# Kernel tuning notes

Hardware: AMD Instinct MI355X
Metric: run time of the kernel (lower is better)

The kernel has to match this reference:

```python
import jax, jax.numpy as jnp
import numpy as np

B, N, F = 32, 64, 128          # batch, num_nodes, n_in_node
K, H, M, NH = 4, 256, 256, 256 # edge_types, msg_hid, msg_out, n_hid
E = N * (N - 1)                # fully-connected directed edges = 4032


def setup_inputs() -> dict:
    key = jax.random.key(0)
    ks = jax.random.split(key, 12)
    inputs = jax.random.normal(ks[0], (B, N, F), dtype=jnp.float32)
    # soft edge-type assignment per edge (rows sum to 1, as in NRI)
    rel_type = jax.nn.softmax(jax.random.normal(ks[1], (B, E, K), dtype=jnp.float32), axis=-1)
    # one-hot receiver/sender matrices for all i != j pairs
    idx = np.array([(i, j) for i in range(N) for j in range(N) if i != j], dtype=np.int64)
    eye = np.eye(N, dtype=np.float32)
    rel_rec = jnp.asarray(eye[idx[:, 0]])   # [E, N]
    rel_send = jnp.asarray(eye[idx[:, 1]])  # [E, N]
    # per-edge-type message MLP weights (stacked over K): y = x @ W + b
    W1 = jax.random.normal(ks[2], (K, 2 * F, H), dtype=jnp.float32) / np.sqrt(2 * F)
    b1 = jnp.zeros((K, H), dtype=jnp.float32)
    W2 = jax.random.normal(ks[3], (K, H, M), dtype=jnp.float32) / np.sqrt(H)
    b2 = jnp.zeros((K, M), dtype=jnp.float32)
    # output MLP
    Wo1 = jax.random.normal(ks[4], (F + M, NH), dtype=jnp.float32) / np.sqrt(F + M)
    bo1 = jnp.zeros((NH,), dtype=jnp.float32)
    Wo2 = jax.random.normal(ks[5], (NH, NH), dtype=jnp.float32) / np.sqrt(NH)
    bo2 = jnp.zeros((NH,), dtype=jnp.float32)
    Wo3 = jax.random.normal(ks[6], (NH, F), dtype=jnp.float32) / np.sqrt(NH)
    bo3 = jnp.zeros((F,), dtype=jnp.float32)
    return {"inputs": inputs, "rel_type": rel_type, "rel_rec": rel_rec, "rel_send": rel_send,
            "W1": W1, "b1": b1, "W2": W2, "b2": b2,
            "Wo1": Wo1, "bo1": bo1, "Wo2": Wo2, "bo2": bo2, "Wo3": Wo3, "bo3": bo3}


def reference(inputs, rel_type, rel_rec, rel_send, W1, b1, W2, b2, Wo1, bo1, Wo2, bo2, Wo3, bo3):
    # gather node states to edges via one-hot matmul (as in the source)
    receivers = jnp.einsum('en,bnf->bef', rel_rec, inputs)   # [B,E,F]
    senders = jnp.einsum('en,bnf->bef', rel_send, inputs)    # [B,E,F]
    pre_msg = jnp.concatenate([receivers, senders], axis=-1)  # [B,E,2F]
    # per-edge-type 2-layer ReLU MLP, batched over the K edge types
    h = jax.nn.relu(jnp.einsum('bef,kfh->bkeh', pre_msg, W1) + b1[:, None, :])  # [B,K,E,H]
    msg = jax.nn.relu(jnp.einsum('bkeh,khm->bkem', h, W2) + b2[:, None, :])     # [B,K,E,M]
    # mask by soft edge type and accumulate over types (dropout p=0 -> identity)
    all_msgs = jnp.einsum('bkem,bek->bem', msg, rel_type)     # [B,E,M]
    # scatter-aggregate messages to receiver nodes via one-hot matmul
    agg_msgs = jnp.einsum('en,bem->bnm', rel_rec, all_msgs)   # [B,N,M]
    aug = jnp.concatenate([inputs, agg_msgs], axis=-1)        # [B,N,F+M]
    p = jax.nn.relu(aug @ Wo1 + bo1)
    p = jax.nn.relu(p @ Wo2 + bo2)
    p = p @ Wo3 + bo3
    return inputs + p
```

## Files before the change

kernel.cpp:

```cpp
#include <hip/hip_runtime.h>


#define B_ 32
#define N_ 64
#define F_ 128
#define K_ 4
#define E_ 4032

#define WS_W2T 0u
#define WS_R   524288u
#define WS_S   4718592u
#define WS_AGG 8912896u

typedef unsigned short u16;
typedef u16    u16x4  __attribute__((ext_vector_type(4)));
typedef u16    u16x8  __attribute__((ext_vector_type(8)));
typedef __bf16 bf16x8 __attribute__((ext_vector_type(8)));
typedef float  f32x4  __attribute__((ext_vector_type(4)));
typedef float  f32x16 __attribute__((ext_vector_type(16)));

__device__ __forceinline__ u16 f2bf(float f) {
    unsigned u; __builtin_memcpy(&u, &f, 4);
    return (u16)((u + 0x7FFFu + ((u >> 16) & 1u)) >> 16);
}
__device__ __forceinline__ float bf2f(u16 u) {
    unsigned v = ((unsigned)u) << 16;
    float f; __builtin_memcpy(&f, &v, 4); return f;
}
__device__ __forceinline__ void gl_lds16(const u16* g, u16* l) {
    __builtin_amdgcn_global_load_lds(
        (const __attribute__((address_space(1))) void*)g,
        (__attribute__((address_space(3))) void*)l, 16, 0, 0);
}

#define LBAR() do { \
    asm volatile("s_waitcnt lgkmcnt(0)" ::: "memory"); \
    __builtin_amdgcn_s_barrier(); \
    __builtin_amdgcn_sched_barrier(0); \
} while (0)

__global__ __launch_bounds__(256) void prep_rs_kernel(
    const float* __restrict__ W2, const float* __restrict__ x,
    const float* __restrict__ W1, const float* __restrict__ b1,
    u16* __restrict__ W2t, u16* __restrict__ R, u16* __restrict__ S)
{
    __shared__ u16 ldsA[64 * 136];
    __shared__ u16 ldsW[32 * 136];
    const int tid = threadIdx.x;

    if (blockIdx.x < 1024) {
        unsigned gid = blockIdx.x * 256u + tid;
        unsigned chunk = gid >> 13, r = gid & 8191u;
        unsigned g = r >> 11, n = (r >> 3) & 255u, e = r & 7u;
        unsigned k = chunk >> 3, kc = chunk & 7u, ks2 = g >> 1, lhh = g & 1u;
        unsigned kk = kc * 32u + ks2 * 16u + lhh * 8u + e;
        W2t[gid] = f2bf(W2[(k * 256u + kk) * 256u + n]);
        return;
    }

    const int lane = tid & 63, w = tid >> 6;
    const int quad = lane >> 4, mloc = lane & 15;
    const int bx = blockIdx.x - 1024;
    const int k = bx >> 6, half = (bx >> 5) & 1, b = bx & 31;

    for (int idx = tid; idx < 2048; idx += 256) {
        int row = idx >> 5, c4 = idx & 31;
        f32x4 v = *(const f32x4*)&x[(b * 64 + row) * 128 + c4 * 4];
        u16x4 o;
#pragma unroll
        for (int e = 0; e < 4; ++e) o[e] = f2bf(v[e]);
        *(u16x4*)&ldsA[row * 136 + c4 * 4] = o;
    }
    __syncthreads();

    bf16x8 aF[4];
#pragma unroll
    for (int ks = 0; ks < 4; ++ks)
        aF[ks] = *(const bf16x8*)&ldsA[(w * 16 + mloc) * 136 + quad * 8 + ks * 32];

    u16* dst = half ? S : R;
    for (int c = 0; c < 8; ++c) {
        __syncthreads();
        for (int idx = tid; idx < 4096; idx += 256) {
            int n = idx & 31, f = idx >> 5;
            ldsW[n * 136 + f] = f2bf(W1[(k * 256 + half * 128 + f) * 256 + c * 32 + n]);
        }
        __syncthreads();
#pragma unroll
        for (int nt = 0; nt < 2; ++nt) {
            f32x4 acc = (f32x4){0.f, 0.f, 0.f, 0.f};
            const int boff = (nt * 16 + mloc) * 136 + quad * 8;
#pragma unroll
            for (int ks = 0; ks < 4; ++ks)
                acc = __builtin_amdgcn_mfma_f32_16x16x32_bf16(
                    aF[ks], *(const bf16x8*)&ldsW[boff + ks * 32], acc, 0, 0, 0);
            const int n = c * 32 + nt * 16 + mloc;
            const float bias = half ? 0.f : b1[k * 256 + n];
#pragma unroll
            for (int r = 0; r < 4; ++r) {
                int row = w * 16 + quad * 4 + r;
                dst[(size_t)(k * 2048 + b * 64 + row) * 256 + n] = f2bf(acc[r] + bias);
            }
        }
    }
}

__global__ __launch_bounds__(256, 2) void edge6_kernel(
    const u16* __restrict__ R, const u16* __restrict__ S,
    const float* __restrict__ rel, const u16* __restrict__ W2t,
    const float* __restrict__ b2, u16* __restrict__ aggb)
{
    __shared__ u16   WtS[3][8192];
    __shared__ u16   HS[2][4][128][8];
    __shared__ float Rf[2][4][256];
    __shared__ float rtS[2][4][64];
    __shared__ float b2S[4][256];

    const int tid  = threadIdx.x;
    const int lane = tid & 63;
    const int w    = tid >> 6;
    const int l31  = lane & 31;
    const int lh   = lane >> 5;
    const int bid  = ((blockIdx.x & 7) << 7) | (blockIdx.x >> 3);
    const int b    = bid >> 5;
    const int i0   = (bid & 31) * 2;
    const int brow = tid >> 2;
    const int bc   = tid & 3;

#pragma unroll
    for (int g = 0; g < 4; ++g) {
        gl_lds16(W2t + g * 2048 + w * 512 + lane * 8,        &WtS[0][g * 2048 + w * 512]);
        gl_lds16(W2t + 8192 + g * 2048 + w * 512 + lane * 8, &WtS[1][g * 2048 + w * 512]);
    }
    for (int t = tid; t < 1024; t += 256) ((float*)b2S)[t] = b2[t];
    for (int t = tid; t < 512; t += 256) {
        int recv = t >> 8, rem = t & 255, k = rem >> 6, j = rem & 63;
        int i = i0 + recv;
        float v = 0.f;
        if (j != i) {
            int jj = j - (j > i);
            v = rel[((size_t)(b * E_) + i * 63 + jj) * 4 + k];
        }
        rtS[recv][k][j] = v;
    }
    {
        int recv = tid >> 7, k = (tid >> 5) & 3, e8 = tid & 31;
        u16x8 t8 = *(const u16x8*)&R[((size_t)(k * 2048 + b * 64 + i0 + recv)) * 256 + e8 * 8];
#pragma unroll
        for (int e = 0; e < 8; ++e) Rf[recv][k][e8 * 8 + e] = bf2f(t8[e]);
    }
    u16x8 sv = *(const u16x8*)&S[((size_t)(b * 64 + brow)) * 256 + bc * 8];
    __syncthreads();

    {
#pragma unroll
        for (int recv = 0; recv < 2; ++recv) {
            const float* rp = &Rf[recv][0][bc * 8];
            f32x4 r0 = *(const f32x4*)rp, r1 = *(const f32x4*)(rp + 4);
            bf16x8 o;
#pragma unroll
            for (int e = 0; e < 4; ++e) {
                o[e]     = (__bf16)fmaxf(r0[e] + bf2f(sv[e]),     0.f);
                o[4 + e] = (__bf16)fmaxf(r1[e] + bf2f(sv[4 + e]), 0.f);
            }
            *(bf16x8*)&HS[0][bc][recv * 64 + brow][0] = o;
        }
    }
    LBAR();

    float amsg[2][2] = {{0.f, 0.f}, {0.f, 0.f}};
    f32x16 acc[4][2];
    int sc = 0;

    for (int it = 0; it < 32; ++it) {
        const int kT = it >> 3, kcT = it & 7;
        if (kcT == 0) {
#pragma unroll
            for (int mt = 0; mt < 4; ++mt)
#pragma unroll
                for (int nt = 0; nt < 2; ++nt) acc[mt][nt] = (f32x16)(0.f);
        }
        u16x8 svN;
        if (it < 31) {
            const int kT2 = (it + 1) >> 3, kc2 = (it + 1) & 7;
            svN = *(const u16x8*)&S[((size_t)(kT2 * 2048 + b * 64 + brow)) * 256 + kc2 * 32 + bc * 8];
        }
        if (it < 30) {
            const int s2 = (sc < 1) ? sc + 2 : sc - 1;
            const u16* src = W2t + (size_t)(it + 2) * 8192;
            u16* dstb = &WtS[s2][0];
#pragma unroll
            for (int g = 0; g < 4; ++g)
                gl_lds16(src + g * 2048 + w * 512 + lane * 8, dstb + g * 2048 + w * 512);
        }
        if (it < 30)       { asm volatile("s_waitcnt vmcnt(9)" ::: "memory"); }
        else if (it == 30) { asm volatile("s_waitcnt vmcnt(5)" ::: "memory"); }
        else               { asm volatile("s_waitcnt vmcnt(0)" ::: "memory"); }
        __builtin_amdgcn_sched_barrier(0);

        const u16* buf = WtS[sc];
        const u16(*hs)[128][8] = HS[it & 1];
        __builtin_amdgcn_s_setprio(1);
#pragma unroll
        for (int ks2 = 0; ks2 < 2; ++ks2) {
            bf16x8 A[4], Bv[2];
#pragma unroll
            for (int mt = 0; mt < 4; ++mt)
                A[mt] = *(const bf16x8*)&hs[ks2 * 2 + lh][mt * 32 + l31][0];
#pragma unroll
            for (int nt = 0; nt < 2; ++nt)
                Bv[nt] = *(const bf16x8*)&buf[(ks2 * 2 + lh) * 2048 + (w * 64 + nt * 32 + l31) * 8];
#pragma unroll
            for (int mt = 0; mt < 4; ++mt)
#pragma unroll
                for (int nt = 0; nt < 2; ++nt)
                    acc[mt][nt] = __builtin_amdgcn_mfma_f32_32x32x16_bf16(A[mt], Bv[nt], acc[mt][nt], 0, 0, 0);
        }
        __builtin_amdgcn_s_setprio(0);

        if (it < 31) {
            const int kT2 = (it + 1) >> 3, kc2 = (it + 1) & 7;
            const int db = (it + 1) & 1;
#pragma unroll
            for (int recv = 0; recv < 2; ++recv) {
                const float* rp = &Rf[recv][kT2][kc2 * 32 + bc * 8];
                f32x4 r0 = *(const f32x4*)rp, r1 = *(const f32x4*)(rp + 4);
                bf16x8 o;
#pragma unroll
                for (int e = 0; e < 4; ++e) {
                    o[e]     = (__bf16)fmaxf(r0[e] + bf2f(svN[e]),     0.f);
                    o[4 + e] = (__bf16)fmaxf(r1[e] + bf2f(svN[4 + e]), 0.f);
                }
                *(bf16x8*)&HS[db][bc][recv * 64 + brow][0] = o;
            }
        }
        if (kcT == 7) {
#pragma unroll
            for (int nt = 0; nt < 2; ++nt) {
                const float bias = b2S[kT][w * 64 + nt * 32 + l31];
#pragma unroll
                for (int mt = 0; mt < 4; ++mt) {
                    const int recv = mt >> 1;
                    float s = 0.f;
#pragma unroll
                    for (int rq = 0; rq < 4; ++rq) {
                        f32x4 rt4 = *(const f32x4*)&rtS[recv][kT][(mt & 1) * 32 + rq * 8 + 4 * lh];
#pragma unroll
                        for (int e = 0; e < 4; ++e) {
                            float v = acc[mt][nt][rq * 4 + e] + bias;
                            v = v > 0.f ? v : 0.f;
                            s += rt4[e] * v;
                        }
                    }
                    amsg[recv][nt] += s;
                }
            }
        }
        LBAR();
        sc = (sc < 2) ? sc + 1 : 0;
    }

#pragma unroll
    for (int recv = 0; recv < 2; ++recv)
#pragma unroll
        for (int nt = 0; nt < 2; ++nt) {
            float s = amsg[recv][nt] + __shfl_xor(amsg[recv][nt], 32);
            if (lh == 0)
                aggb[(size_t)(b * 64 + i0 + recv) * 256 + w * 64 + nt * 32 + l31] = f2bf(s);
        }
}

__global__ __launch_bounds__(256) void outmlp3_kernel(
    const float* __restrict__ x, const u16* __restrict__ aggb,
    const float* __restrict__ Wo1, const float* __restrict__ bo1,
    const float* __restrict__ Wo2, const float* __restrict__ bo2,
    const float* __restrict__ Wo3, const float* __restrict__ bo3,
    float* __restrict__ out)
{
    __shared__ u16 wch[4][256][8];
    __shared__ u16 p1S[32 * 264];
    __shared__ u16 p2S[32 * 264];
    const int tid = threadIdx.x, lane = tid & 63, w = tid >> 6;
    const int quad = lane >> 4, mloc = lane & 15;
    const int row0 = blockIdx.x * 32;

    {
        f32x4 acc[2][4];
#pragma unroll
        for (int mt = 0; mt < 2; ++mt)
#pragma unroll
            for (int nt = 0; nt < 4; ++nt) acc[mt][nt] = (f32x4){0.f, 0.f, 0.f, 0.f};
        float wr[32];
#pragma unroll
        for (int g = 0; g < 4; ++g)
#pragma unroll
            for (int e = 0; e < 8; ++e) wr[g * 8 + e] = Wo1[(g * 8 + e) * 256 + tid];
        for (int kk = 0; kk < 12; ++kk) {
            bf16x8 aF[2];
#pragma unroll
            for (int mt = 0; mt < 2; ++mt) {
                const int row = row0 + mt * 16 + mloc;
                if (kk < 4) {
                    u16x8 t;
#pragma unroll
                    for (int e = 0; e < 8; ++e) t[e] = f2bf(x[row * 128 + kk * 32 + quad * 8 + e]);
                    __builtin_memcpy(&aF[mt], &t, 16);
                } else {
                    aF[mt] = *(const bf16x8*)&aggb[(size_t)row * 256 + (kk - 4) * 32 + quad * 8];
                }
            }
#pragma unroll
            for (int g = 0; g < 4; ++g) {
                u16x8 o;
#pragma unroll
                for (int e = 0; e < 8; ++e) o[e] = f2bf(wr[g * 8 + e]);
                *(u16x8*)&wch[g][tid][0] = o;
            }
            if (kk + 1 < 12) {
#pragma unroll
                for (int g = 0; g < 4; ++g)
#pragma unroll
                    for (int e = 0; e < 8; ++e) wr[g * 8 + e] = Wo1[((kk + 1) * 32 + g * 8 + e) * 256 + tid];
            }
            LBAR();
#pragma unroll
            for (int nt = 0; nt < 4; ++nt) {
                bf16x8 bF = *(const bf16x8*)&wch[quad][w * 64 + nt * 16 + mloc][0];
#pragma unroll
                for (int mt = 0; mt < 2; ++mt)
                    acc[mt][nt] = __builtin_amdgcn_mfma_f32_16x16x32_bf16(aF[mt], bF, acc[mt][nt], 0, 0, 0);
            }
            LBAR();
        }
#pragma unroll
        for (int nt = 0; nt < 4; ++nt) {
            const int n = w * 64 + nt * 16 + mloc;
            const float bias = bo1[n];
#pragma unroll
            for (int mt = 0; mt < 2; ++mt)
#pragma unroll
                for (int r = 0; r < 4; ++r) {
                    float v = acc[mt][nt][r] + bias;
                    p1S[(mt * 16 + quad * 4 + r) * 264 + n] = f2bf(v > 0.f ? v : 0.f);
                }
        }
    }
    LBAR();
    {
        f32x4 acc[2][4];
#pragma unroll
        for (int mt = 0; mt < 2; ++mt)
#pragma unroll
            for (int nt = 0; nt < 4; ++nt) acc[mt][nt] = (f32x4){0.f, 0.f, 0.f, 0.f};
        float wr[32];
#pragma unroll
        for (int g = 0; g < 4; ++g)
#pragma unroll
            for (int e = 0; e < 8; ++e) wr[g * 8 + e] = Wo2[(g * 8 + e) * 256 + tid];
        for (int kk = 0; kk < 8; ++kk) {
            bf16x8 aF[2];
#pragma unroll
            for (int mt = 0; mt < 2; ++mt)
                aF[mt] = *(const bf16x8*)&p1S[(mt * 16 + mloc) * 264 + kk * 32 + quad * 8];
#pragma unroll
            for (int g = 0; g < 4; ++g) {
                u16x8 o;
#pragma unroll
                for (int e = 0; e < 8; ++e) o[e] = f2bf(wr[g * 8 + e]);
                *(u16x8*)&wch[g][tid][0] = o;
            }
            if (kk + 1 < 8) {
#pragma unroll
                for (int g = 0; g < 4; ++g)
#pragma unroll
                    for (int e = 0; e < 8; ++e) wr[g * 8 + e] = Wo2[((kk + 1) * 32 + g * 8 + e) * 256 + tid];
            }
            LBAR();
#pragma unroll
            for (int nt = 0; nt < 4; ++nt) {
                bf16x8 bF = *(const bf16x8*)&wch[quad][w * 64 + nt * 16 + mloc][0];
#pragma unroll
                for (int mt = 0; mt < 2; ++mt)
                    acc[mt][nt] = __builtin_amdgcn_mfma_f32_16x16x32_bf16(aF[mt], bF, acc[mt][nt], 0, 0, 0);
            }
            LBAR();
        }
#pragma unroll
        for (int nt = 0; nt < 4; ++nt) {
            const int n = w * 64 + nt * 16 + mloc;
            const float bias = bo2[n];
#pragma unroll
            for (int mt = 0; mt < 2; ++mt)
#pragma unroll
                for (int r = 0; r < 4; ++r) {
                    float v = acc[mt][nt][r] + bias;
                    p2S[(mt * 16 + quad * 4 + r) * 264 + n] = f2bf(v > 0.f ? v : 0.f);
                }
        }
    }
    LBAR();
    {
        f32x4 acc[2][2];
#pragma unroll
        for (int mt = 0; mt < 2; ++mt)
#pragma unroll
            for (int nt = 0; nt < 2; ++nt) acc[mt][nt] = (f32x4){0.f, 0.f, 0.f, 0.f};
        const int sn = tid & 127, sh = tid >> 7;
        float wr[16];
#pragma unroll
        for (int g2 = 0; g2 < 2; ++g2)
#pragma unroll
            for (int e = 0; e < 8; ++e) wr[g2 * 8 + e] = Wo3[((sh * 2 + g2) * 8 + e) * 128 + sn];
        for (int kk = 0; kk < 8; ++kk) {
            bf16x8 aF[2];
#pragma unroll
            for (int mt = 0; mt < 2; ++mt)
                aF[mt] = *(const bf16x8*)&p2S[(mt * 16 + mloc) * 264 + kk * 32 + quad * 8];
#pragma unroll
            for (int g2 = 0; g2 < 2; ++g2) {
                const int g = sh * 2 + g2;
                u16x8 o;
#pragma unroll
                for (int e = 0; e < 8; ++e) o[e] = f2bf(wr[g2 * 8 + e]);
                *(u16x8*)&wch[g][sn][0] = o;
            }
            if (kk + 1 < 8) {
#pragma unroll
                for (int g2 = 0; g2 < 2; ++g2)
#pragma unroll
                    for (int e = 0; e < 8; ++e)
                        wr[g2 * 8 + e] = Wo3[((kk + 1) * 32 + (sh * 2 + g2) * 8 + e) * 128 + sn];
            }
            LBAR();
#pragma unroll
            for (int nt = 0; nt < 2; ++nt) {
                bf16x8 bF = *(const bf16x8*)&wch[quad][w * 32 + nt * 16 + mloc][0];
#pragma unroll
                for (int mt = 0; mt < 2; ++mt)
                    acc[mt][nt] = __builtin_amdgcn_mfma_f32_16x16x32_bf16(aF[mt], bF, acc[mt][nt], 0, 0, 0);
            }
            LBAR();
        }
#pragma unroll
        for (int nt = 0; nt < 2; ++nt) {
            const int n = w * 32 + nt * 16 + mloc;
            const float bias = bo3[n];
#pragma unroll
            for (int mt = 0; mt < 2; ++mt)
#pragma unroll
                for (int r = 0; r < 4; ++r) {
                    const int grow = row0 + mt * 16 + quad * 4 + r;
                    out[grow * 128 + n] = x[grow * 128 + n] + acc[mt][nt][r] + bias;
                }
        }
    }
}

extern "C" void kernel_launch(void* const* d_in, const int* in_sizes, int n_in,
                              void* d_out, int out_size, void* d_ws, size_t ws_size,
                              hipStream_t stream) {
    const float* x   = (const float*)d_in[0];
    const float* rel = (const float*)d_in[1];
    const float* W1  = (const float*)d_in[4];
    const float* b1  = (const float*)d_in[5];
    const float* W2  = (const float*)d_in[6];
    const float* b2  = (const float*)d_in[7];
    const float* Wo1 = (const float*)d_in[8];
    const float* bo1 = (const float*)d_in[9];
    const float* Wo2 = (const float*)d_in[10];
    const float* bo2 = (const float*)d_in[11];
    const float* Wo3 = (const float*)d_in[12];
    const float* bo3 = (const float*)d_in[13];
    float* out = (float*)d_out;

    char* ws = (char*)d_ws;
    u16* W2t  = (u16*)(ws + WS_W2T);
    u16* R    = (u16*)(ws + WS_R);
    u16* S    = (u16*)(ws + WS_S);
    u16* aggb = (u16*)(ws + WS_AGG);

    prep_rs_kernel<<<1280, 256, 0, stream>>>(W2, x, W1, b1, W2t, R, S);
    edge6_kernel<<<1024, 256, 0, stream>>>(R, S, rel, W2t, b2, aggb);
    outmlp3_kernel<<<64, 256, 0, stream>>>(x, aggb, Wo1, bo1, Wo2, bo2, Wo3, bo3, out);
}
```

Measured before the change: 224.2 us.

## Replace triple-buffered W2 prefetch with double-buffering and plain syncthreads

The edge kernel drops from a three-stage LDS ring for W2 tiles, prefetched two iterations ahead with explicit vmcnt waits, to a two-stage double buffer prefetched one iteration ahead. Synchronisation now uses __syncthreads instead of the custom barrier, and the s_setprio hints and sched_barrier are removed. The b2 bias is read from global memory rather than staged in LDS. This cuts LDS use, which may help occupancy or simplify scheduling. The cost is less latency hiding for the global-to-LDS loads, and the full barrier likely waits on all outstanding loads each iteration.

```diff
diff --git a/kernel.cpp b/kernel.cpp
--- a/kernel.cpp
+++ b/kernel.cpp
@@ -105,16 +105,15 @@
     }
 }
 
-__global__ __launch_bounds__(256, 2) void edge6_kernel(
+__global__ __launch_bounds__(256, 2) void edge7_kernel(
     const u16* __restrict__ R, const u16* __restrict__ S,
     const float* __restrict__ rel, const u16* __restrict__ W2t,
     const float* __restrict__ b2, u16* __restrict__ aggb)
 {
-    __shared__ u16   WtS[3][8192];
+    __shared__ u16   WtS[2][8192];
     __shared__ u16   HS[2][4][128][8];
     __shared__ float Rf[2][4][256];
     __shared__ float rtS[2][4][64];
-    __shared__ float b2S[4][256];
 
     const int tid  = threadIdx.x;
     const int lane = tid & 63;
@@ -127,12 +126,13 @@
     const int brow = tid >> 2;
     const int bc   = tid & 3;
 
-#pragma unroll
-    for (int g = 0; g < 4; ++g) {
-        gl_lds16(W2t + g * 2048 + w * 512 + lane * 8,        &WtS[0][g * 2048 + w * 512]);
-        gl_lds16(W2t + 8192 + g * 2048 + w * 512 + lane * 8, &WtS[1][g * 2048 + w * 512]);
-    }
-    for (int t = tid; t < 1024; t += 256) ((float*)b2S)[t] = b2[t];
+    {
+        const u16* src = W2t + w * 2048;
+        u16* dst = &WtS[0][w * 2048];
+#pragma unroll
+        for (int it2 = 0; it2 < 4; ++it2)
+            gl_lds16(src + it2 * 512 + lane * 8, dst + it2 * 512);
+    }
     for (int t = tid; t < 512; t += 256) {
         int recv = t >> 8, rem = t & 255, k = rem >> 6, j = rem & 63;
         int i = i0 + recv;
@@ -166,11 +166,10 @@
             *(bf16x8*)&HS[0][bc][recv * 64 + brow][0] = o;
         }
     }
-    LBAR();
+    __syncthreads();
 
     float amsg[2][2] = {{0.f, 0.f}, {0.f, 0.f}};
     f32x16 acc[4][2];
-    int sc = 0;
 
     for (int it = 0; it < 32; ++it) {
         const int kT = it >> 3, kcT = it & 7;
@@ -182,25 +181,16 @@
         }
         u16x8 svN;
         if (it < 31) {
+            const u16* src = W2t + (size_t)(it + 1) * 8192 + w * 2048;
+            u16* dst = &WtS[(it + 1) & 1][w * 2048];
+#pragma unroll
+            for (int it2 = 0; it2 < 4; ++it2)
+                gl_lds16(src + it2 * 512 + lane * 8, dst + it2 * 512);
             const int kT2 = (it + 1) >> 3, kc2 = (it + 1) & 7;
             svN = *(const u16x8*)&S[((size_t)(kT2 * 2048 + b * 64 + brow)) * 256 + kc2 * 32 + bc * 8];
         }
-        if (it < 30) {
-            const int s2 = (sc < 1) ? sc + 2 : sc - 1;
-            const u16* src = W2t + (size_t)(it + 2) * 8192;
-            u16* dstb = &WtS[s2][0];
-#pragma unroll
-            for (int g = 0; g < 4; ++g)
-                gl_lds16(src + g * 2048 + w * 512 + lane * 8, dstb + g * 2048 + w * 512);
-        }
-        if (it < 30)       { asm volatile("s_waitcnt vmcnt(9)" ::: "memory"); }
-        else if (it == 30) { asm volatile("s_waitcnt vmcnt(5)" ::: "memory"); }
-        else               { asm volatile("s_waitcnt vmcnt(0)" ::: "memory"); }
-        __builtin_amdgcn_sched_barrier(0);
-
-        const u16* buf = WtS[sc];
+        const u16* buf = WtS[it & 1];
         const u16(*hs)[128][8] = HS[it & 1];
-        __builtin_amdgcn_s_setprio(1);
 #pragma unroll
         for (int ks2 = 0; ks2 < 2; ++ks2) {
             bf16x8 A[4], Bv[2];
@@ -216,8 +206,6 @@
                 for (int nt = 0; nt < 2; ++nt)
                     acc[mt][nt] = __builtin_amdgcn_mfma_f32_32x32x16_bf16(A[mt], Bv[nt], acc[mt][nt], 0, 0, 0);
         }
-        __builtin_amdgcn_s_setprio(0);
-
         if (it < 31) {
             const int kT2 = (it + 1) >> 3, kc2 = (it + 1) & 7;
             const int db = (it + 1) & 1;
@@ -237,7 +225,7 @@
         if (kcT == 7) {
 #pragma unroll
             for (int nt = 0; nt < 2; ++nt) {
-                const float bias = b2S[kT][w * 64 + nt * 32 + l31];
+                const float bias = b2[kT * 256 + w * 64 + nt * 32 + l31];
 #pragma unroll
                 for (int mt = 0; mt < 4; ++mt) {
                     const int recv = mt >> 1;
@@ -256,8 +244,7 @@
                 }
             }
         }
-        LBAR();
-        sc = (sc < 2) ? sc + 1 : 0;
+        __syncthreads();
     }
 
 #pragma unroll
@@ -480,6 +467,6 @@
     u16* aggb = (u16*)(ws + WS_AGG);
 
     prep_rs_kernel<<<1280, 256, 0, stream>>>(W2, x, W1, b1, W2t, R, S);
-    edge6_kernel<<<1024, 256, 0, stream>>>(R, S, rel, W2t, b2, aggb);
+    edge7_kernel<<<1024, 256, 0, stream>>>(R, S, rel, W2t, b2, aggb);
     outmlp3_kernel<<<64, 256, 0, stream>>>(x, aggb, Wo1, bo1, Wo2, bo2, Wo3, bo3, out);
 }
```

New measurement: 207.3 us. 7.5% less time.
